# Kernel tuning notes

Measured on AMD Instinct MI355X. Metric: run time of the kernel, lower is better.

The kernel has to match this reference:

```python
import jax, jax.numpy as jnp
import numpy as np

EPS = 1e-5

def _ln(x, g, b):
    mu = x.mean(-1, keepdims=True)
    var = ((x - mu) ** 2).mean(-1, keepdims=True)
    return (x - mu) / jnp.sqrt(var + EPS) * g + b

def setup_inputs() -> dict:
    key = jax.random.key(0)
    ks = jax.random.split(key, 24)
    B, S, I, H, D, F = 64, 512, 32, 64, 128, 256
    def w(k, shape, fan_in):
        return jax.random.uniform(k, shape, jnp.float32, -1.0, 1.0) / np.sqrt(fan_in)
    return {
        'x': jax.random.normal(ks[0], (B, S, I), jnp.float32),
        'W_ih': w(ks[1], (H, I), H), 'b_ih': w(ks[2], (H,), H),
        'W_hh': w(ks[3], (H, H), H), 'b_hh': w(ks[4], (H,), H),
        'Wp': w(ks[5], (D, H), H), 'bp': w(ks[6], (D,), H),
        'Wqkv': w(ks[7], (3 * D, D), D), 'bqkv': jnp.zeros((3 * D,), jnp.float32),
        'Wo': w(ks[8], (D, D), D), 'bo': jnp.zeros((D,), jnp.float32),
        'g1': jnp.ones((D,), jnp.float32), 'be1': jnp.zeros((D,), jnp.float32),
        'W1': w(ks[9], (F, D), D), 'b1': w(ks[10], (F,), D),
        'W2': w(ks[11], (D, F), F), 'b2': w(ks[12], (D,), F),
        'g2': jnp.ones((D,), jnp.float32), 'be2': jnp.zeros((D,), jnp.float32),
        'gn': jnp.ones((D,), jnp.float32), 'bn': jnp.zeros((D,), jnp.float32),
        'Wf': w(ks[13], (I, D), D), 'bf': w(ks[14], (I,), D),
    }

def reference(x, W_ih, b_ih, W_hh, b_hh, Wp, bp, Wqkv, bqkv, Wo, bo,
              g1, be1, W1, b1, W2, b2, g2, be2, gn, bn, Wf, bf):
    B, S, I = x.shape
    H = W_ih.shape[0]
    D = Wp.shape[0]
    nh = 8
    hd = D // nh

    # RNNCell tanh recurrence over time (sequential, vectorized over batch)
    xs = jnp.swapaxes(x, 0, 1)  # (S, B, I)
    def step(h, x_t):
        h = jnp.tanh(x_t @ W_ih.T + b_ih + h @ W_hh.T + b_hh)
        return h, h
    _, hs = jax.lax.scan(step, jnp.zeros((B, H), x.dtype), xs)  # (S, B, H)

    proj = hs @ Wp.T + bp  # (S, B, D)

    # TransformerEncoderLayer (post-norm, relu), dropout = identity (eval)
    qkv = proj @ Wqkv.T + bqkv  # (S, B, 3D)
    q, k, v = jnp.split(qkv, 3, axis=-1)
    q = q.reshape(S, B, nh, hd)
    k = k.reshape(S, B, nh, hd)
    v = v.reshape(S, B, nh, hd)
    scores = jnp.einsum('sbhd,tbhd->bhst', q, k) / np.sqrt(hd)
    attn = jax.nn.softmax(scores, axis=-1)
    ctx = jnp.einsum('bhst,tbhd->sbhd', attn, v).reshape(S, B, D)
    attn_out = ctx @ Wo.T + bo
    x1 = _ln(proj + attn_out, g1, be1)
    ff = jax.nn.relu(x1 @ W1.T + b1) @ W2.T + b2
    x2 = _ln(x1 + ff, g2, be2)

    out = _ln(x2 + proj, gn, bn)
    pooled = out.mean(axis=0)  # (B, D)
    return jnp.tanh(pooled @ Wf.T + bf)
```

## Files before the change

kernel.cpp:

```cpp
#include <hip/hip_runtime.h>
#include <hip/hip_bf16.h>

#define BB 64
#define SS 512
#define II 32
#define HH 64
#define DD 128
#define FF 256
#define NHEAD 8
#define HDIM 16
#define NTOK (SS*BB)

typedef short bf16x8 __attribute__((ext_vector_type(8)));
typedef float f32x4  __attribute__((ext_vector_type(4)));

__device__ __forceinline__ float fast_tanh(float x) {
    float ax = fabsf(x);
    float e = __expf(-2.0f * ax);
    float r = (1.0f - e) * __builtin_amdgcn_rcpf(1.0f + e);
    return copysignf(r, x);
}

__device__ __forceinline__ float bcast(float v, int lane) {
    return __int_as_float(__builtin_amdgcn_readlane(__float_as_int(v), lane));
}

__device__ __forceinline__ short f2bf(float x) {
    unsigned u = __float_as_uint(x);
    return (short)((u + 0x7FFFu + ((u >> 16) & 1u)) >> 16);
}

__global__ __launch_bounds__(256) void k_xw(const float* __restrict__ x,
                                            const float* __restrict__ W_ih,
                                            const float* __restrict__ b_ih,
                                            const float* __restrict__ b_hh,
                                            float* __restrict__ xw) {
    int idx = blockIdx.x * 256 + threadIdx.x;
    int j  = idx & (HH - 1);
    int sb = idx >> 6;
    int s  = sb >> 6;
    int b  = sb & (BB - 1);
    const float* xr = x + (b * SS + s) * II;
    const float* wr = W_ih + j * II;
    float acc = b_ih[j] + b_hh[j];
    #pragma unroll
    for (int k = 0; k < II; k += 4) {
        float4 xv = *(const float4*)(xr + k);
        float4 wv = *(const float4*)(wr + k);
        acc += xv.x * wv.x + xv.y * wv.y + xv.z * wv.z + xv.w * wv.w;
    }
    xw[idx] = acc;
}

__global__ __launch_bounds__(64, 1) void k_rnn(const float* __restrict__ xw,
                                               const float* __restrict__ W_hh,
                                               float* __restrict__ hs) {
    int b = blockIdx.x;
    int j = threadIdx.x;
    float w[HH];
    #pragma unroll
    for (int k = 0; k < HH; k++) w[k] = W_hh[j * HH + k];

    float hv = 0.0f;
    float xv0 = xw[(0 * BB + b) * HH + j];
    float xv1 = xw[(1 * BB + b) * HH + j];
    for (int t = 0; t < SS; t++) {
        int tn = (t < SS - 2) ? t + 2 : t;
        float xnext = xw[(tn * BB + b) * HH + j];
        float a0 = xv0, a1 = 0.f, a2 = 0.f, a3 = 0.f;
        #pragma unroll
        for (int k = 0; k < HH; k += 4) {
            a0 = fmaf(w[k + 0], bcast(hv, k + 0), a0);
            a1 = fmaf(w[k + 1], bcast(hv, k + 1), a1);
            a2 = fmaf(w[k + 2], bcast(hv, k + 2), a2);
            a3 = fmaf(w[k + 3], bcast(hv, k + 3), a3);
        }
        hv = fast_tanh((a0 + a1) + (a2 + a3));
        hs[(t * BB + b) * HH + j] = hv;
        xv0 = xv1;
        xv1 = xnext;
    }
}

template<int K, bool RELU>
__global__ __launch_bounds__(256) void k_gemm_mfma(const float* __restrict__ A,
                                                   const float* __restrict__ W,
                                                   const float* __restrict__ bias,
                                                   float* __restrict__ C, int N) {
    __shared__ short As[128 * 40];
    __shared__ short Ws[64 * 40];
    int tid = threadIdx.x;
    int wid = tid >> 6, lane = tid & 63;
    int col = lane & 15, quad = lane >> 4;
    int rowBase = blockIdx.x * 128, colBase = blockIdx.y * 64;

    f32x4 acc[2][4];
    #pragma unroll
    for (int nt = 0; nt < 4; nt++) {
        float bv = bias[colBase + nt * 16 + col];
        #pragma unroll
        for (int mt = 0; mt < 2; mt++) {
            acc[mt][nt][0] = bv; acc[mt][nt][1] = bv;
            acc[mt][nt][2] = bv; acc[mt][nt][3] = bv;
        }
    }

    int arow = tid >> 1, akb = (tid & 1) * 16;
    int wrow = tid >> 2, wkb = (tid & 3) * 8;

    for (int kb = 0; kb < K; kb += 32) {
        {
            const float4* ap = (const float4*)(A + (size_t)(rowBase + arow) * K + kb + akb);
            float4 v0 = ap[0], v1 = ap[1], v2 = ap[2], v3 = ap[3];
            short t0[8], t1[8];
            t0[0]=f2bf(v0.x); t0[1]=f2bf(v0.y); t0[2]=f2bf(v0.z); t0[3]=f2bf(v0.w);
            t0[4]=f2bf(v1.x); t0[5]=f2bf(v1.y); t0[6]=f2bf(v1.z); t0[7]=f2bf(v1.w);
            t1[0]=f2bf(v2.x); t1[1]=f2bf(v2.y); t1[2]=f2bf(v2.z); t1[3]=f2bf(v2.w);
            t1[4]=f2bf(v3.x); t1[5]=f2bf(v3.y); t1[6]=f2bf(v3.z); t1[7]=f2bf(v3.w);
            *(int4*)&As[arow * 40 + akb]     = *(int4*)t0;
            *(int4*)&As[arow * 40 + akb + 8] = *(int4*)t1;
        }
        {
            const float4* wp = (const float4*)(W + (size_t)(colBase + wrow) * K + kb + wkb);
            float4 v0 = wp[0], v1 = wp[1];
            short t0[8];
            t0[0]=f2bf(v0.x); t0[1]=f2bf(v0.y); t0[2]=f2bf(v0.z); t0[3]=f2bf(v0.w);
            t0[4]=f2bf(v1.x); t0[5]=f2bf(v1.y); t0[6]=f2bf(v1.z); t0[7]=f2bf(v1.w);
            *(int4*)&Ws[wrow * 40 + wkb] = *(int4*)t0;
        }
        __syncthreads();

        bf16x8 af[2], wf[4];
        #pragma unroll
        for (int mt = 0; mt < 2; mt++)
            af[mt] = *(const bf16x8*)&As[(wid * 32 + mt * 16 + col) * 40 + quad * 8];
        #pragma unroll
        for (int nt = 0; nt < 4; nt++)
            wf[nt] = *(const bf16x8*)&Ws[(nt * 16 + col) * 40 + quad * 8];
        #pragma unroll
        for (int mt = 0; mt < 2; mt++)
            #pragma unroll
            for (int nt = 0; nt < 4; nt++)
                acc[mt][nt] = __builtin_amdgcn_mfma_f32_16x16x32_bf16(af[mt], wf[nt], acc[mt][nt], 0, 0, 0);
        __syncthreads();
    }

    #pragma unroll
    for (int mt = 0; mt < 2; mt++) {
        #pragma unroll
        for (int r = 0; r < 4; r++) {
            int m = rowBase + wid * 32 + mt * 16 + quad * 4 + r;
            float* crow = C + (size_t)m * N + colBase;
            #pragma unroll
            for (int nt = 0; nt < 4; nt++) {
                float v = acc[mt][nt][r];
                if (RELU) v = fmaxf(v, 0.f);
                crow[nt * 16 + col] = v;
            }
        }
    }
}

__global__ __launch_bounds__(256, 2) void k_attn(const float* __restrict__ qkv,
                                                 float* __restrict__ ctx) {
    int bh = blockIdx.x;
    int b = bh >> 3, h = bh & 7;
    __shared__ short Klds[SS * 32];
    __shared__ short Vt[HDIM][SS];
    __shared__ short Pb[4][2][16 * 64];
    int tid = threadIdx.x;

    for (int t = tid; t < SS; t += 256) {
        const float* base = qkv + (size_t)(t * BB + b) * 384 + h * 16;
        float4 k0 = *(const float4*)(base + 128);
        float4 k1 = *(const float4*)(base + 132);
        float4 k2 = *(const float4*)(base + 136);
        float4 k3 = *(const float4*)(base + 140);
        float4 v0 = *(const float4*)(base + 256);
        float4 v1 = *(const float4*)(base + 260);
        float4 v2 = *(const float4*)(base + 264);
        float4 v3 = *(const float4*)(base + 268);
        short* kd = &Klds[t * 32];
        kd[0]=f2bf(k0.x); kd[1]=f2bf(k0.y); kd[2]=f2bf(k0.z); kd[3]=f2bf(k0.w);
        kd[4]=f2bf(k1.x); kd[5]=f2bf(k1.y); kd[6]=f2bf(k1.z); kd[7]=f2bf(k1.w);
        kd[8]=f2bf(k2.x); kd[9]=f2bf(k2.y); kd[10]=f2bf(k2.z); kd[11]=f2bf(k2.w);
        kd[12]=f2bf(k3.x); kd[13]=f2bf(k3.y); kd[14]=f2bf(k3.z); kd[15]=f2bf(k3.w);
        *(int4*)&kd[16] = make_int4(0, 0, 0, 0);
        *(int4*)&kd[24] = make_int4(0, 0, 0, 0);
        Vt[0][t]=f2bf(v0.x);  Vt[1][t]=f2bf(v0.y);  Vt[2][t]=f2bf(v0.z);  Vt[3][t]=f2bf(v0.w);
        Vt[4][t]=f2bf(v1.x);  Vt[5][t]=f2bf(v1.y);  Vt[6][t]=f2bf(v1.z);  Vt[7][t]=f2bf(v1.w);
        Vt[8][t]=f2bf(v2.x);  Vt[9][t]=f2bf(v2.y);  Vt[10][t]=f2bf(v2.z); Vt[11][t]=f2bf(v2.w);
        Vt[12][t]=f2bf(v3.x); Vt[13][t]=f2bf(v3.y); Vt[14][t]=f2bf(v3.z); Vt[15][t]=f2bf(v3.w);
    }
    __syncthreads();

    int wid = tid >> 6, lane = tid & 63;
    int col = lane & 15, quad = lane >> 4;
    const float qscale = 0.25f * 1.44269504f;

    for (int sub = 0; sub < 8; sub++) {
        int q0 = wid * 128 + sub * 16;

        bf16x8 qf = (bf16x8)(short)0;
        if (quad < 2) {
            const float* qsrc = qkv + (size_t)((q0 + col) * BB + b) * 384 + h * 16 + quad * 8;
            float4 qa = *(const float4*)qsrc;
            float4 qb = *(const float4*)(qsrc + 4);
            qf[0]=f2bf(qa.x*qscale); qf[1]=f2bf(qa.y*qscale);
            qf[2]=f2bf(qa.z*qscale); qf[3]=f2bf(qa.w*qscale);
            qf[4]=f2bf(qb.x*qscale); qf[5]=f2bf(qb.y*qscale);
            qf[6]=f2bf(qb.z*qscale); qf[7]=f2bf(qb.w*qscale);
        }

        f32x4 S[32];
        #pragma unroll
        for (int kt = 0; kt < 32; kt++) {
            bf16x8 kf = *(const bf16x8*)&Klds[(kt * 16 + col) * 32 + quad * 8];
            f32x4 z = {0.f, 0.f, 0.f, 0.f};
            S[kt] = __builtin_amdgcn_mfma_f32_16x16x32_bf16(qf, kf, z, 0, 0, 0);
        }

        float mx[4], sm[4];
        #pragma unroll
        for (int r = 0; r < 4; r++) {
            float m = S[0][r];
            #pragma unroll
            for (int kt = 1; kt < 32; kt++) m = fmaxf(m, S[kt][r]);
            #pragma unroll
            for (int off = 1; off < 16; off <<= 1) m = fmaxf(m, __shfl_xor(m, off, 64));
            mx[r] = m;
        }
        #pragma unroll
        for (int r = 0; r < 4; r++) {
            float s = 0.f;
            #pragma unroll
            for (int kt = 0; kt < 32; kt++) {
                float p = exp2f(S[kt][r] - mx[r]);
                S[kt][r] = p;
                s += p;
            }
            #pragma unroll
            for (int off = 1; off < 16; off <<= 1) s += __shfl_xor(s, off, 64);
            sm[r] = s;
        }

        f32x4 O = {0.f, 0.f, 0.f, 0.f};
        #pragma unroll
        for (int c = 0; c < 8; c++) {
            short* pbuf = &Pb[wid][c & 1][0];
            #pragma unroll
            for (int kk = 0; kk < 4; kk++) {
                int kt = c * 4 + kk;
                #pragma unroll
                for (int r = 0; r < 4; r++)
                    pbuf[(4 * quad + r) * 64 + kk * 16 + col] = f2bf(S[kt][r]);
            }
            #pragma unroll
            for (int half = 0; half < 2; half++) {
                int tbase = c * 64 + half * 32;
                bf16x8 pf = *(const bf16x8*)&pbuf[col * 64 + half * 32 + quad * 8];
                bf16x8 vf = *(const bf16x8*)&Vt[col][tbase + quad * 8];
                O = __builtin_amdgcn_mfma_f32_16x16x32_bf16(pf, vf, O, 0, 0, 0);
            }
        }

        #pragma unroll
        for (int r = 0; r < 4; r++) {
            float inv = __builtin_amdgcn_rcpf(sm[r]);
            int q = q0 + 4 * quad + r;
            ctx[(size_t)(q * BB + b) * DD + h * 16 + col] = O[r] * inv;
        }
    }
}

__global__ __launch_bounds__(256) void k_add_ln(const float* __restrict__ a,
                                                const float* __restrict__ bres,
                                                const float* __restrict__ g,
                                                const float* __restrict__ be,
                                                float* __restrict__ out) {
    int row = blockIdx.x * 4 + (threadIdx.x >> 6);
    int lane = threadIdx.x & 63;
    const float* ar = a + (size_t)row * DD;
    const float* br = bres + (size_t)row * DD;
    float v0 = ar[lane] + br[lane];
    float v1 = ar[lane + 64] + br[lane + 64];
    float sum = v0 + v1;
    #pragma unroll
    for (int off = 32; off; off >>= 1) sum += __shfl_xor(sum, off, 64);
    float mu = sum * (1.0f / 128.0f);
    float d0 = v0 - mu, d1 = v1 - mu;
    float vs = d0 * d0 + d1 * d1;
    #pragma unroll
    for (int off = 32; off; off >>= 1) vs += __shfl_xor(vs, off, 64);
    float rstd = rsqrtf(vs * (1.0f / 128.0f) + 1e-5f);
    float* orow = out + (size_t)row * DD;
    orow[lane]      = d0 * rstd * g[lane] + be[lane];
    orow[lane + 64] = d1 * rstd * g[lane + 64] + be[lane + 64];
}

__global__ __launch_bounds__(128) void k_pool(const float* __restrict__ out_ln,
                                              float* __restrict__ pooled) {
    int b = blockIdx.x;
    int d = threadIdx.x;
    float sum = 0.f;
    #pragma unroll 8
    for (int s = 0; s < SS; s++) sum += out_ln[(size_t)(s * BB + b) * DD + d];
    pooled[b * DD + d] = sum * (1.0f / SS);
}

__global__ __launch_bounds__(64) void k_final(const float* __restrict__ pooled,
                                              const float* __restrict__ Wf,
                                              const float* __restrict__ bf,
                                              float* __restrict__ out) {
    int idx = blockIdx.x * 64 + threadIdx.x;
    int b = idx >> 5, i = idx & 31;
    const float* pr = pooled + b * DD;
    const float* wr = Wf + i * DD;
    float acc = bf[i];
    #pragma unroll
    for (int k = 0; k < DD; k += 4) {
        float4 p = *(const float4*)(pr + k);
        float4 w = *(const float4*)(wr + k);
        acc += p.x * w.x + p.y * w.y + p.z * w.z + p.w * w.w;
    }
    out[idx] = fast_tanh(acc);
}

extern "C" void kernel_launch(void* const* d_in, const int* in_sizes, int n_in,
                              void* d_out, int out_size, void* d_ws, size_t ws_size,
                              hipStream_t stream) {
    const float* x    = (const float*)d_in[0];
    const float* W_ih = (const float*)d_in[1];
    const float* b_ih = (const float*)d_in[2];
    const float* W_hh = (const float*)d_in[3];
    const float* b_hh = (const float*)d_in[4];
    const float* Wp   = (const float*)d_in[5];
    const float* bp   = (const float*)d_in[6];
    const float* Wqkv = (const float*)d_in[7];
    const float* bqkv = (const float*)d_in[8];
    const float* Wo   = (const float*)d_in[9];
    const float* bo   = (const float*)d_in[10];
    const float* g1   = (const float*)d_in[11];
    const float* be1  = (const float*)d_in[12];
    const float* W1   = (const float*)d_in[13];
    const float* b1   = (const float*)d_in[14];
    const float* W2   = (const float*)d_in[15];
    const float* b2   = (const float*)d_in[16];
    const float* g2   = (const float*)d_in[17];
    const float* be2  = (const float*)d_in[18];
    const float* gn   = (const float*)d_in[19];
    const float* bn   = (const float*)d_in[20];
    const float* Wf   = (const float*)d_in[21];
    const float* bf   = (const float*)d_in[22];
    float* out = (float*)d_out;
    float* ws  = (float*)d_ws;

    float* proj     = ws + 0;
    float* qkv      = ws + 4194304;
    float* outln    = ws + 4194304;
    float* x2       = ws + 8388608;
    float* xw       = ws + 16777216;
    float* hsbuf    = ws + 18874368;
    float* ctx      = ws + 16777216;
    float* ff2      = ws + 16777216;
    float* x1       = ws + 20971520;
    float* attn_out = ws + 25165824;
    float* ff1      = ws + 25165824;
    float* pooled   = ws + 33554432;

    k_xw<<<8192, 256, 0, stream>>>(x, W_ih, b_ih, b_hh, xw);
    k_rnn<<<64, 64, 0, stream>>>(xw, W_hh, hsbuf);
    k_gemm_mfma<64,  false><<<dim3(256, 2), 256, 0, stream>>>(hsbuf, Wp, bp, proj, 128);
    k_gemm_mfma<128, false><<<dim3(256, 6), 256, 0, stream>>>(proj, Wqkv, bqkv, qkv, 384);
    k_attn<<<512, 256, 0, stream>>>(qkv, ctx);
    k_gemm_mfma<128, false><<<dim3(256, 2), 256, 0, stream>>>(ctx, Wo, bo, attn_out, 128);
    k_add_ln<<<8192, 256, 0, stream>>>(proj, attn_out, g1, be1, x1);
    k_gemm_mfma<128, true ><<<dim3(256, 4), 256, 0, stream>>>(x1, W1, b1, ff1, 256);
    k_gemm_mfma<256, false><<<dim3(256, 2), 256, 0, stream>>>(ff1, W2, b2, ff2, 128);
    k_add_ln<<<8192, 256, 0, stream>>>(x1, ff2, g2, be2, x2);
    k_add_ln<<<8192, 256, 0, stream>>>(x2, proj, gn, bn, outln);
    k_pool<<<64, 128, 0, stream>>>(outln, pooled);
    k_final<<<32, 64, 0, stream>>>(pooled, Wf, bf, out);
}
```

Measured before the change: 469.0 us.

## Fuse output GEMMs with residual LayerNorm, merge pool+final, batch RNN stores

Adds a full-width (N=128) MFMA GEMM kernel whose epilogue applies the residual add and one or two LayerNorms. It replaces the Wo GEMM plus add_ln, and the W2 GEMM plus two add_ln passes, which removes several full-tensor round trips through global memory. Pool and final projection are merged into one kernel with a two-way split over the sequence. The RNN buffers 64 timesteps of hidden state in LDS and writes them as coalesced float4 rows, in place of one scalar store per step. The cost is higher register pressure from 16 accumulators per thread, and only 256 blocks for the fused GEMMs.

```diff
diff --git a/kernel.cpp b/kernel.cpp
--- a/kernel.cpp
+++ b/kernel.cpp
@@ -61,6 +61,8 @@
     #pragma unroll
     for (int k = 0; k < HH; k++) w[k] = W_hh[j * HH + k];
 
+    __shared__ float hbuf[64 * 68];
+
     float hv = 0.0f;
     float xv0 = xw[(0 * BB + b) * HH + j];
     float xv1 = xw[(1 * BB + b) * HH + j];
@@ -76,7 +78,17 @@
             a3 = fmaf(w[k + 3], bcast(hv, k + 3), a3);
         }
         hv = fast_tanh((a0 + a1) + (a2 + a3));
-        hs[(t * BB + b) * HH + j] = hv;
+        hbuf[(t & 63) * 68 + j] = hv;
+        if ((t & 63) == 63) {
+            int tg = t - 63 + j;
+            const float* src = &hbuf[j * 68];
+            float* dst = hs + (size_t)(tg * BB + b) * HH;
+            #pragma unroll
+            for (int c = 0; c < 16; c++) {
+                float4 v4 = *(const float4*)&src[c * 4];
+                *(float4*)&dst[c * 4] = v4;
+            }
+        }
         xv0 = xv1;
         xv1 = xnext;
     }
@@ -157,6 +169,137 @@
                 if (RELU) v = fmaxf(v, 0.f);
                 crow[nt * 16 + col] = v;
             }
+        }
+    }
+}
+
+template<int K, int NLN>
+__global__ __launch_bounds__(256) void k_gemm_ln(const float* __restrict__ A,
+                                                 const float* __restrict__ W,
+                                                 const float* __restrict__ bias,
+                                                 const float* __restrict__ res1,
+                                                 const float* __restrict__ g1v,
+                                                 const float* __restrict__ be1v,
+                                                 const float* __restrict__ res2,
+                                                 const float* __restrict__ g2v,
+                                                 const float* __restrict__ be2v,
+                                                 float* __restrict__ out) {
+    __shared__ short As[128 * 40];
+    __shared__ short Ws[128 * 40];
+    int tid = threadIdx.x;
+    int wid = tid >> 6, lane = tid & 63;
+    int col = lane & 15, quad = lane >> 4;
+    int rowBase = blockIdx.x * 128;
+
+    f32x4 acc[2][8];
+    #pragma unroll
+    for (int nt = 0; nt < 8; nt++) {
+        float bv = bias[nt * 16 + col];
+        #pragma unroll
+        for (int mt = 0; mt < 2; mt++) {
+            acc[mt][nt][0] = bv; acc[mt][nt][1] = bv;
+            acc[mt][nt][2] = bv; acc[mt][nt][3] = bv;
+        }
+    }
+
+    int arow = tid >> 1, akb = (tid & 1) * 16;
+
+    for (int kb = 0; kb < K; kb += 32) {
+        {
+            const float4* ap = (const float4*)(A + (size_t)(rowBase + arow) * K + kb + akb);
+            float4 v0 = ap[0], v1 = ap[1], v2 = ap[2], v3 = ap[3];
+            short t0[8], t1[8];
+            t0[0]=f2bf(v0.x); t0[1]=f2bf(v0.y); t0[2]=f2bf(v0.z); t0[3]=f2bf(v0.w);
+            t0[4]=f2bf(v1.x); t0[5]=f2bf(v1.y); t0[6]=f2bf(v1.z); t0[7]=f2bf(v1.w);
+            t1[0]=f2bf(v2.x); t1[1]=f2bf(v2.y); t1[2]=f2bf(v2.z); t1[3]=f2bf(v2.w);
+            t1[4]=f2bf(v3.x); t1[5]=f2bf(v3.y); t1[6]=f2bf(v3.z); t1[7]=f2bf(v3.w);
+            *(int4*)&As[arow * 40 + akb]     = *(int4*)t0;
+            *(int4*)&As[arow * 40 + akb + 8] = *(int4*)t1;
+        }
+        {
+            const float4* wp = (const float4*)(W + (size_t)arow * K + kb + akb);
+            float4 v0 = wp[0], v1 = wp[1], v2 = wp[2], v3 = wp[3];
+            short t0[8], t1[8];
+            t0[0]=f2bf(v0.x); t0[1]=f2bf(v0.y); t0[2]=f2bf(v0.z); t0[3]=f2bf(v0.w);
+            t0[4]=f2bf(v1.x); t0[5]=f2bf(v1.y); t0[6]=f2bf(v1.z); t0[7]=f2bf(v1.w);
+            t1[0]=f2bf(v2.x); t1[1]=f2bf(v2.y); t1[2]=f2bf(v2.z); t1[3]=f2bf(v2.w);
+            t1[4]=f2bf(v3.x); t1[5]=f2bf(v3.y); t1[6]=f2bf(v3.z); t1[7]=f2bf(v3.w);
+            *(int4*)&Ws[arow * 40 + akb]     = *(int4*)t0;
+            *(int4*)&Ws[arow * 40 + akb + 8] = *(int4*)t1;
+        }
+        __syncthreads();
+
+        bf16x8 af[2], wf[8];
+        #pragma unroll
+        for (int mt = 0; mt < 2; mt++)
+            af[mt] = *(const bf16x8*)&As[(wid * 32 + mt * 16 + col) * 40 + quad * 8];
+        #pragma unroll
+        for (int nt = 0; nt < 8; nt++)
+            wf[nt] = *(const bf16x8*)&Ws[(nt * 16 + col) * 40 + quad * 8];
+        #pragma unroll
+        for (int mt = 0; mt < 2; mt++)
+            #pragma unroll
+            for (int nt = 0; nt < 8; nt++)
+                acc[mt][nt] = __builtin_amdgcn_mfma_f32_16x16x32_bf16(af[mt], wf[nt], acc[mt][nt], 0, 0, 0);
+        __syncthreads();
+    }
+
+    float ga[8], ba[8], gb[8], bb[8];
+    #pragma unroll
+    for (int nt = 0; nt < 8; nt++) {
+        ga[nt] = g1v[nt * 16 + col]; ba[nt] = be1v[nt * 16 + col];
+        if (NLN == 2) { gb[nt] = g2v[nt * 16 + col]; bb[nt] = be2v[nt * 16 + col]; }
+    }
+
+    #pragma unroll
+    for (int mt = 0; mt < 2; mt++) {
+        #pragma unroll
+        for (int r = 0; r < 4; r++) {
+            int m = rowBase + wid * 32 + mt * 16 + quad * 4 + r;
+            const float* rr1 = res1 + (size_t)m * DD;
+            float v[8];
+            float s = 0.f;
+            #pragma unroll
+            for (int nt = 0; nt < 8; nt++) {
+                v[nt] = acc[mt][nt][r] + rr1[nt * 16 + col];
+                s += v[nt];
+            }
+            #pragma unroll
+            for (int off = 1; off < 16; off <<= 1) s += __shfl_xor(s, off, 64);
+            float mu = s * (1.0f / 128.0f);
+            float vs = 0.f;
+            #pragma unroll
+            for (int nt = 0; nt < 8; nt++) { v[nt] -= mu; vs += v[nt] * v[nt]; }
+            #pragma unroll
+            for (int off = 1; off < 16; off <<= 1) vs += __shfl_xor(vs, off, 64);
+            float rstd = rsqrtf(vs * (1.0f / 128.0f) + 1e-5f);
+            #pragma unroll
+            for (int nt = 0; nt < 8; nt++) v[nt] = v[nt] * rstd * ga[nt] + ba[nt];
+
+            if (NLN == 2) {
+                const float* rr2 = res2 + (size_t)m * DD;
+                float s2 = 0.f;
+                #pragma unroll
+                for (int nt = 0; nt < 8; nt++) {
+                    v[nt] += rr2[nt * 16 + col];
+                    s2 += v[nt];
+                }
+                #pragma unroll
+                for (int off = 1; off < 16; off <<= 1) s2 += __shfl_xor(s2, off, 64);
+                float mu2 = s2 * (1.0f / 128.0f);
+                float vs2 = 0.f;
+                #pragma unroll
+                for (int nt = 0; nt < 8; nt++) { v[nt] -= mu2; vs2 += v[nt] * v[nt]; }
+                #pragma unroll
+                for (int off = 1; off < 16; off <<= 1) vs2 += __shfl_xor(vs2, off, 64);
+                float rstd2 = rsqrtf(vs2 * (1.0f / 128.0f) + 1e-5f);
+                #pragma unroll
+                for (int nt = 0; nt < 8; nt++) v[nt] = v[nt] * rstd2 * gb[nt] + bb[nt];
+            }
+
+            float* orow = out + (size_t)m * DD;
+            #pragma unroll
+            for (int nt = 0; nt < 8; nt++) orow[nt * 16 + col] = v[nt];
         }
     }
 }
@@ -273,57 +416,35 @@
     }
 }
 
-__global__ __launch_bounds__(256) void k_add_ln(const float* __restrict__ a,
-                                                const float* __restrict__ bres,
-                                                const float* __restrict__ g,
-                                                const float* __restrict__ be,
-                                                float* __restrict__ out) {
-    int row = blockIdx.x * 4 + (threadIdx.x >> 6);
-    int lane = threadIdx.x & 63;
-    const float* ar = a + (size_t)row * DD;
-    const float* br = bres + (size_t)row * DD;
-    float v0 = ar[lane] + br[lane];
-    float v1 = ar[lane + 64] + br[lane + 64];
-    float sum = v0 + v1;
-    #pragma unroll
-    for (int off = 32; off; off >>= 1) sum += __shfl_xor(sum, off, 64);
-    float mu = sum * (1.0f / 128.0f);
-    float d0 = v0 - mu, d1 = v1 - mu;
-    float vs = d0 * d0 + d1 * d1;
-    #pragma unroll
-    for (int off = 32; off; off >>= 1) vs += __shfl_xor(vs, off, 64);
-    float rstd = rsqrtf(vs * (1.0f / 128.0f) + 1e-5f);
-    float* orow = out + (size_t)row * DD;
-    orow[lane]      = d0 * rstd * g[lane] + be[lane];
-    orow[lane + 64] = d1 * rstd * g[lane + 64] + be[lane + 64];
-}
-
-__global__ __launch_bounds__(128) void k_pool(const float* __restrict__ out_ln,
-                                              float* __restrict__ pooled) {
+__global__ __launch_bounds__(256) void k_poolfinal(const float* __restrict__ outln,
+                                                   const float* __restrict__ Wf,
+                                                   const float* __restrict__ bfv,
+                                                   float* __restrict__ out) {
     int b = blockIdx.x;
-    int d = threadIdx.x;
-    float sum = 0.f;
+    int tid = threadIdx.x;
+    __shared__ float part[256];
+    __shared__ float pooled[128];
+    int d = tid & 127, half = tid >> 7;
+    float s = 0.f;
+    int s0 = half * 256;
     #pragma unroll 8
-    for (int s = 0; s < SS; s++) sum += out_ln[(size_t)(s * BB + b) * DD + d];
-    pooled[b * DD + d] = sum * (1.0f / SS);
-}
-
-__global__ __launch_bounds__(64) void k_final(const float* __restrict__ pooled,
-                                              const float* __restrict__ Wf,
-                                              const float* __restrict__ bf,
-                                              float* __restrict__ out) {
-    int idx = blockIdx.x * 64 + threadIdx.x;
-    int b = idx >> 5, i = idx & 31;
-    const float* pr = pooled + b * DD;
-    const float* wr = Wf + i * DD;
-    float acc = bf[i];
-    #pragma unroll
-    for (int k = 0; k < DD; k += 4) {
-        float4 p = *(const float4*)(pr + k);
-        float4 w = *(const float4*)(wr + k);
-        acc += p.x * w.x + p.y * w.y + p.z * w.z + p.w * w.w;
-    }
-    out[idx] = fast_tanh(acc);
+    for (int si = s0; si < s0 + 256; si++)
+        s += outln[(size_t)(si * BB + b) * DD + d];
+    part[tid] = s;
+    __syncthreads();
+    if (tid < 128) pooled[tid] = (part[tid] + part[tid + 128]) * (1.0f / SS);
+    __syncthreads();
+    if (tid < 32) {
+        const float* wr = Wf + tid * DD;
+        float acc = bfv[tid];
+        #pragma unroll
+        for (int k = 0; k < DD; k += 4) {
+            float4 wv = *(const float4*)(wr + k);
+            acc += pooled[k] * wv.x + pooled[k + 1] * wv.y
+                 + pooled[k + 2] * wv.z + pooled[k + 3] * wv.w;
+        }
+        out[b * 32 + tid] = fast_tanh(acc);
+    }
 }
 
 extern "C" void kernel_launch(void* const* d_in, const int* in_sizes, int n_in,
@@ -355,30 +476,24 @@
     float* out = (float*)d_out;
     float* ws  = (float*)d_ws;
 
-    float* proj     = ws + 0;
-    float* qkv      = ws + 4194304;
-    float* outln    = ws + 4194304;
-    float* x2       = ws + 8388608;
-    float* xw       = ws + 16777216;
-    float* hsbuf    = ws + 18874368;
-    float* ctx      = ws + 16777216;
-    float* ff2      = ws + 16777216;
-    float* x1       = ws + 20971520;
-    float* attn_out = ws + 25165824;
-    float* ff1      = ws + 25165824;
-    float* pooled   = ws + 33554432;
+    float* proj   = ws + 0;
+    float* qkv    = ws + 4194304;
+    float* outln  = ws + 4194304;
+    float* xw     = ws + 16777216;
+    float* hsbuf  = ws + 18874368;
+    float* ctx    = ws + 16777216;
+    float* x1     = ws + 20971520;
+    float* ff1    = ws + 25165824;
 
     k_xw<<<8192, 256, 0, stream>>>(x, W_ih, b_ih, b_hh, xw);
     k_rnn<<<64, 64, 0, stream>>>(xw, W_hh, hsbuf);
     k_gemm_mfma<64,  false><<<dim3(256, 2), 256, 0, stream>>>(hsbuf, Wp, bp, proj, 128);
     k_gemm_mfma<128, false><<<dim3(256, 6), 256, 0, stream>>>(proj, Wqkv, bqkv, qkv, 384);
     k_attn<<<512, 256, 0, stream>>>(qkv, ctx);
-    k_gemm_mfma<128, false><<<dim3(256, 2), 256, 0, stream>>>(ctx, Wo, bo, attn_out, 128);
-    k_add_ln<<<8192, 256, 0, stream>>>(proj, attn_out, g1, be1, x1);
+    k_gemm_ln<128, 1><<<256, 256, 0, stream>>>(ctx, Wo, bo, proj, g1, be1,
+                                               nullptr, nullptr, nullptr, x1);
     k_gemm_mfma<128, true ><<<dim3(256, 4), 256, 0, stream>>>(x1, W1, b1, ff1, 256);
-    k_gemm_mfma<256, false><<<dim3(256, 2), 256, 0, stream>>>(ff1, W2, b2, ff2, 128);
-    k_add_ln<<<8192, 256, 0, stream>>>(x1, ff2, g2, be2, x2);
-    k_add_ln<<<8192, 256, 0, stream>>>(x2, proj, gn, bn, outln);
-    k_pool<<<64, 128, 0, stream>>>(outln, pooled);
-    k_final<<<32, 64, 0, stream>>>(pooled, Wf, bf, out);
-}
+    k_gemm_ln<256, 2><<<256, 256, 0, stream>>>(ff1, W2, b2, x1, g2, be2,
+                                               proj, gn, bn, outln);
+    k_poolfinal<<<64, 256, 0, stream>>>(outln, Wf, bf, out);
+}
```

Measured after the change: 457.2 us. 1.03x faster.
